# Kernel tuning notes

Measured on AMD Instinct MI355X. Metric: run time of the kernel, lower is better.

## Reference

```python
import jax, jax.numpy as jnp
import numpy as np

BN_EPS = 1e-5
NORM_EPS = 1e-12


def setup_inputs() -> dict:
    key = jax.random.key(0)
    ks = jax.random.split(key, 7)
    B, N, D, K, G = 64, 2048, 512, 64, 16
    init_sc = 1.0 / np.sqrt(D)
    return {
        "x": jax.random.normal(ks[0], (B, N, D), dtype=jnp.float32),
        "clusters": init_sc * jax.random.normal(ks[1], (D, K + G), dtype=jnp.float32),
        "clusters2": init_sc * jax.random.normal(ks[2], (1, D, K), dtype=jnp.float32),
        "bn_weight": jax.random.uniform(ks[3], (K + G,), dtype=jnp.float32, minval=0.5, maxval=1.5),
        "bn_bias": 0.1 * jax.random.normal(ks[4], (K + G,), dtype=jnp.float32),
        "running_mean": 0.1 * jax.random.normal(ks[5], (K + G,), dtype=jnp.float32),
        "running_var": jax.random.uniform(ks[6], (K + G,), dtype=jnp.float32, minval=0.5, maxval=1.5),
    }


def reference(x, clusters, clusters2, bn_weight, bn_bias, running_mean, running_var):
    # x: [B, N, D]; clusters: [D, K+G]; clusters2: [1, D, K]
    K = clusters2.shape[-1]
    # fused projection + BN (inference/affine form) + softmax over all K+G clusters
    scale = bn_weight * jax.lax.rsqrt(running_var + BN_EPS)          # [K+G]
    logits = jnp.einsum("bnd,dk->bnk", x, clusters)                  # [B, N, K+G]
    logits = (logits - running_mean) * scale + bn_bias
    assignment = jax.nn.softmax(logits, axis=-1)[..., :K]            # [B, N, K]
    # VLAD aggregation
    a_sum = jnp.sum(assignment, axis=1, keepdims=True)               # [B, 1, K]
    a = a_sum.transpose(0, 2, 1)[:, None, :, 0] * 0                  # placeholder avoided; compute directly below
    a = a_sum * clusters2.transpose(0, 2, 1)[..., None][..., 0].transpose(0, 2, 1) if False else a_sum.swapaxes(1, 2)[..., None][..., 0]  # not used
    a = jnp.einsum("bok,odk->bdk", a_sum, clusters2)                 # [B, D, K]
    vlad = jnp.einsum("bnd,bnk->bdk", x, assignment) - a             # [B, D, K]
    # intra-normalize over D
    vlad = vlad / jnp.maximum(jnp.linalg.norm(vlad, axis=1, keepdims=True), NORM_EPS)
    vlad = vlad.reshape(vlad.shape[0], -1)                           # [B, D*K]
    vlad = vlad / jnp.maximum(jnp.linalg.norm(vlad, axis=-1, keepdims=True), NORM_EPS)
    return vlad
```

## Files before the change

kernel.cpp:

```cpp
#include <hip/hip_runtime.h>
#include <hip/hip_bf16.h>
#include <math.h>
#include <string.h>

#define BN 131072

typedef __attribute__((ext_vector_type(8))) short bf16x8;
typedef __attribute__((ext_vector_type(4))) float f32x4;

__device__ __forceinline__ unsigned short f2bf(float f) {
    unsigned int u = __float_as_uint(f);
    u += 0x7fffu + ((u >> 16) & 1u);
    return (unsigned short)(u >> 16);
}

__device__ __forceinline__ unsigned int pk_bf16(float a, float b) {
    __hip_bfloat162 h = __float22bfloat162_rn(float2{a, b});
    unsigned int u;
    memcpy(&u, &h, 4);
    return u;
}

__global__ __launch_bounds__(256) void prep(
    const float* __restrict__ clusters, const float* __restrict__ bnw,
    const float* __restrict__ bnb, const float* __restrict__ rm,
    const float* __restrict__ rv,
    unsigned short* __restrict__ cT, float* __restrict__ bnadd)
{
    int i = blockIdx.x * 256 + threadIdx.x;
    int d = i / 80;
    int kg = i - d * 80;
    float mul = bnw[kg] * rsqrtf(rv[kg] + 1e-5f);
    cT[kg * 512 + d] = f2bf(clusters[i] * mul);
    if (i < 80) bnadd[i] = bnb[i] - rm[i] * mul;
}

__global__ __launch_bounds__(256) void pass_a(
    const float* __restrict__ x, const unsigned short* __restrict__ cT,
    const float* __restrict__ bnadd,
    unsigned short* __restrict__ assignT, float* __restrict__ a_sum)
{
    __shared__ unsigned short xs[64 * 136];
    __shared__ unsigned short cs[80 * 136];

    const int tid = threadIdx.x;
    const int w = tid >> 6, lane = tid & 63;
    const int q = lane >> 4, m = lane & 15;
    const int rowbase = blockIdx.x * 64;
    const int b = rowbase >> 11;

    f32x4 acc[5];
#pragma unroll
    for (int t = 0; t < 5; ++t) acc[t] = (f32x4){0.f, 0.f, 0.f, 0.f};

    for (int c = 0; c < 4; ++c) {
#pragma unroll
        for (int r = 0; r < 8; ++r) {
            int i = tid + 256 * r;
            int row = i >> 5, dd = (i & 31) * 4;
            float4 v = *(const float4*)(x + (size_t)(rowbase + row) * 512 + c * 128 + dd);
            uint2 p = { pk_bf16(v.x, v.y), pk_bf16(v.z, v.w) };
            *(uint2*)&xs[row * 136 + dd] = p;
        }
#pragma unroll
        for (int r = 0; r < 10; ++r) {
            int i = tid + 256 * r;
            int kg = i >> 5, dd = (i & 31) * 4;
            *(ushort4*)&cs[kg * 136 + dd] = *(const ushort4*)(cT + kg * 512 + c * 128 + dd);
        }
        __syncthreads();
#pragma unroll
        for (int ks = 0; ks < 4; ++ks) {
            bf16x8 a = *(const bf16x8*)&xs[(w * 16 + m) * 136 + ks * 32 + q * 8];
#pragma unroll
            for (int t = 0; t < 5; ++t) {
                bf16x8 bb = *(const bf16x8*)&cs[(m + 16 * t) * 136 + ks * 32 + q * 8];
                acc[t] = __builtin_amdgcn_mfma_f32_16x16x32_bf16(a, bb, acc[t], 0, 0, 0);
            }
        }
        __syncthreads();
    }

    float addv[5];
#pragma unroll
    for (int t = 0; t < 5; ++t) addv[t] = bnadd[m + 16 * t];

    float e[5][4], rs4[4];
#pragma unroll
    for (int i = 0; i < 4; ++i) {
        float v[5];
#pragma unroll
        for (int t = 0; t < 5; ++t) v[t] = acc[t][i] + addv[t];
        float mx = v[0];
#pragma unroll
        for (int t = 1; t < 5; ++t) mx = fmaxf(mx, v[t]);
        mx = fmaxf(mx, __shfl_xor(mx, 1, 64));
        mx = fmaxf(mx, __shfl_xor(mx, 2, 64));
        mx = fmaxf(mx, __shfl_xor(mx, 4, 64));
        mx = fmaxf(mx, __shfl_xor(mx, 8, 64));
        float sum = 0.f;
#pragma unroll
        for (int t = 0; t < 5; ++t) { e[t][i] = __expf(v[t] - mx); sum += e[t][i]; }
        sum += __shfl_xor(sum, 1, 64);
        sum += __shfl_xor(sum, 2, 64);
        sum += __shfl_xor(sum, 4, 64);
        sum += __shfl_xor(sum, 8, 64);
        rs4[i] = 1.0f / sum;
    }

    const int n0 = rowbase + w * 16 + q * 4;
#pragma unroll
    for (int t = 0; t < 4; ++t) {
        float a0 = e[t][0] * rs4[0], a1 = e[t][1] * rs4[1];
        float a2 = e[t][2] * rs4[2], a3 = e[t][3] * rs4[3];
        uint2 h = { pk_bf16(a0, a1), pk_bf16(a2, a3) };
        *(uint2*)(assignT + (size_t)(m + 16 * t) * BN + n0) = h;
        float as = a0 + a1 + a2 + a3;
        as += __shfl_xor(as, 16, 64);
        as += __shfl_xor(as, 32, 64);
        if (lane < 16) atomicAdd(&a_sum[b * 64 + m + 16 * t], as);
    }
}

__global__ __launch_bounds__(256) void pass_b(
    const float* __restrict__ x, const unsigned short* __restrict__ assignT,
    const float* __restrict__ a_sum, const float* __restrict__ clusters2,
    float* __restrict__ vlad, float* __restrict__ colssq)
{
    __shared__ unsigned short xs2[64 * 130];
    __shared__ unsigned short as2[64 * 72];

    const int tid = threadIdx.x;
    const int w = tid >> 6, lane = tid & 63;
    const int q = lane >> 4, m = lane & 15;
    const int dt = blockIdx.x;
    const int b = blockIdx.y;

    f32x4 acc[4];
#pragma unroll
    for (int t = 0; t < 4; ++t) acc[t] = (f32x4){0.f, 0.f, 0.f, 0.f};

    for (int nc = 0; nc < 2048; nc += 64) {
#pragma unroll
        for (int r = 0; r < 4; ++r) {
            int i = tid + 256 * r;
            int nl = i >> 4, dd = (i & 15) * 4;
            float4 v = *(const float4*)(x + (size_t)(b * 2048 + nc + nl) * 512 + dt * 64 + dd);
            *(unsigned int*)&xs2[nl * 130 + dd]     = pk_bf16(v.x, v.y);
            *(unsigned int*)&xs2[nl * 130 + dd + 2] = pk_bf16(v.z, v.w);
        }
#pragma unroll
        for (int r = 0; r < 4; ++r) {
            int i = tid + 256 * r;
            int kc = i >> 4, nl4 = (i & 15) * 4;
            *(ushort4*)&as2[kc * 72 + nl4] =
                *(const ushort4*)(assignT + (size_t)kc * BN + b * 2048 + nc + nl4);
        }
        __syncthreads();
#pragma unroll
        for (int ks = 0; ks < 2; ++ks) {
            union { unsigned short u[8]; bf16x8 v; } af;
            const int dcol = w * 16 + m;
#pragma unroll
            for (int j = 0; j < 8; ++j)
                af.u[j] = xs2[(ks * 32 + q * 8 + j) * 130 + dcol];
#pragma unroll
            for (int nt = 0; nt < 4; ++nt) {
                bf16x8 bb = *(const bf16x8*)&as2[(nt * 16 + m) * 72 + ks * 32 + q * 8];
                acc[nt] = __builtin_amdgcn_mfma_f32_16x16x32_bf16(af.v, bb, acc[nt], 0, 0, 0);
            }
        }
        __syncthreads();
    }

    const int d0 = dt * 64 + w * 16 + q * 4;
#pragma unroll
    for (int nt = 0; nt < 4; ++nt) {
        int kc = nt * 16 + m;
        float asv = a_sum[b * 64 + kc];
        float ss = 0.f;
#pragma unroll
        for (int i = 0; i < 4; ++i) {
            int d = d0 + i;
            float v = acc[nt][i] - asv * clusters2[d * 64 + kc];
            vlad[((size_t)b * 512 + d) * 64 + kc] = v;
            ss += v * v;
        }
        ss += __shfl_xor(ss, 16, 64);
        ss += __shfl_xor(ss, 32, 64);
        if (lane < 16) atomicAdd(&colssq[b * 64 + kc], ss);
    }
}

__global__ __launch_bounds__(256) void pass_c(
    const float* __restrict__ vlad, const float* __restrict__ colssq,
    float* __restrict__ out)
{
    __shared__ float sc[65];
    const int b = blockIdx.y, seg = blockIdx.x, tid = threadIdx.x;

    if (tid < 64) {
        float css = colssq[b * 64 + tid];
        float invc = 1.0f / fmaxf(sqrtf(css), 1e-12f);
        sc[tid] = invc;
        float ns = css * invc * invc;
        ns += __shfl_xor(ns, 1, 64);
        ns += __shfl_xor(ns, 2, 64);
        ns += __shfl_xor(ns, 4, 64);
        ns += __shfl_xor(ns, 8, 64);
        ns += __shfl_xor(ns, 16, 64);
        ns += __shfl_xor(ns, 32, 64);
        if (tid == 0) sc[64] = 1.0f / fmaxf(sqrtf(ns), 1e-12f);
    }
    __syncthreads();
    const float invr = sc[64];

#pragma unroll
    for (int r = 0; r < 4; ++r) {
        int i4 = seg * 1024 + r * 256 + tid;
        float4 v = *(const float4*)(vlad + (size_t)b * 32768 + (size_t)i4 * 4);
        int c0 = (i4 & 15) * 4;
        float4 o;
        o.x = v.x * sc[c0 + 0] * invr;
        o.y = v.y * sc[c0 + 1] * invr;
        o.z = v.z * sc[c0 + 2] * invr;
        o.w = v.w * sc[c0 + 3] * invr;
        *(float4*)(out + (size_t)b * 32768 + (size_t)i4 * 4) = o;
    }
}

extern "C" void kernel_launch(void* const* d_in, const int* in_sizes, int n_in,
                              void* d_out, int out_size, void* d_ws, size_t ws_size,
                              hipStream_t stream)
{
    const float* x         = (const float*)d_in[0];
    const float* clusters  = (const float*)d_in[1];
    const float* clusters2 = (const float*)d_in[2];
    const float* bn_w      = (const float*)d_in[3];
    const float* bn_b      = (const float*)d_in[4];
    const float* rmean     = (const float*)d_in[5];
    const float* rvar      = (const float*)d_in[6];
    float* out = (float*)d_out;

    char* ws = (char*)d_ws;
    float* a_sum            = (float*)(ws + 0);
    float* colssq           = (float*)(ws + 16384);
    float* bnadd            = (float*)(ws + 32768);
    unsigned short* cT      = (unsigned short*)(ws + 65536);
    unsigned short* assignT = (unsigned short*)(ws + 262144);
    float* vlad             = (float*)(ws + 262144 + 16777216);

    hipMemsetAsync(ws, 0, 32768, stream);

    prep<<<160, 256, 0, stream>>>(clusters, bn_w, bn_b, rmean, rvar, cT, bnadd);
    pass_a<<<2048, 256, 0, stream>>>(x, cT, bnadd, assignT, a_sum);
    pass_b<<<dim3(8, 64), 256, 0, stream>>>(x, assignT, a_sum, clusters2, vlad, colssq);
    pass_c<<<dim3(8, 64), 256, 0, stream>>>(vlad, colssq, out);
}
```

Baseline: 527.8 us.

## Prefetch next tiles into registers and split pass_b over N with partial reduction

Both GEMM passes now load the next chunk of x and cluster/assignment data into registers while the current chunk is consumed from shared memory, so global load latency overlaps with MFMA work. pass_b is split into two N-halves via a z grid dimension, which doubles the block count from 512 to 1024 for better occupancy on the GPU. The halves write partial results to a new workspace buffer. A new pass_c1 kernel sums the two partials, writes vlad and accumulates column sums of squares. This adds one kernel launch, extra partial-buffer traffic, and higher register pressure from the prefetch arrays.

Result: faster. 449.8 us (-14.8%).

```diff
diff --git a/kernel.cpp b/kernel.cpp
--- a/kernel.cpp
+++ b/kernel.cpp
@@ -53,22 +53,53 @@
 #pragma unroll
     for (int t = 0; t < 5; ++t) acc[t] = (f32x4){0.f, 0.f, 0.f, 0.f};
 
+    float4  vx[8];
+    ushort4 vc[10];
+
+#pragma unroll
+    for (int r = 0; r < 8; ++r) {
+        int i = tid + 256 * r;
+        int row = i >> 5, dd = (i & 31) * 4;
+        vx[r] = *(const float4*)(x + (size_t)(rowbase + row) * 512 + dd);
+    }
+#pragma unroll
+    for (int r = 0; r < 10; ++r) {
+        int i = tid + 256 * r;
+        int kg = i >> 5, dd = (i & 31) * 4;
+        vc[r] = *(const ushort4*)(cT + kg * 512 + dd);
+    }
+
     for (int c = 0; c < 4; ++c) {
 #pragma unroll
         for (int r = 0; r < 8; ++r) {
             int i = tid + 256 * r;
             int row = i >> 5, dd = (i & 31) * 4;
-            float4 v = *(const float4*)(x + (size_t)(rowbase + row) * 512 + c * 128 + dd);
-            uint2 p = { pk_bf16(v.x, v.y), pk_bf16(v.z, v.w) };
+            uint2 p = { pk_bf16(vx[r].x, vx[r].y), pk_bf16(vx[r].z, vx[r].w) };
             *(uint2*)&xs[row * 136 + dd] = p;
         }
 #pragma unroll
         for (int r = 0; r < 10; ++r) {
             int i = tid + 256 * r;
             int kg = i >> 5, dd = (i & 31) * 4;
-            *(ushort4*)&cs[kg * 136 + dd] = *(const ushort4*)(cT + kg * 512 + c * 128 + dd);
+            *(ushort4*)&cs[kg * 136 + dd] = vc[r];
         }
         __syncthreads();
+
+        if (c < 3) {
+#pragma unroll
+            for (int r = 0; r < 8; ++r) {
+                int i = tid + 256 * r;
+                int row = i >> 5, dd = (i & 31) * 4;
+                vx[r] = *(const float4*)(x + (size_t)(rowbase + row) * 512 + (c + 1) * 128 + dd);
+            }
+#pragma unroll
+            for (int r = 0; r < 10; ++r) {
+                int i = tid + 256 * r;
+                int kg = i >> 5, dd = (i & 31) * 4;
+                vc[r] = *(const ushort4*)(cT + kg * 512 + (c + 1) * 128 + dd);
+            }
+        }
+
 #pragma unroll
         for (int ks = 0; ks < 4; ++ks) {
             bf16x8 a = *(const bf16x8*)&xs[(w * 16 + m) * 136 + ks * 32 + q * 8];
@@ -125,7 +156,7 @@
 __global__ __launch_bounds__(256) void pass_b(
     const float* __restrict__ x, const unsigned short* __restrict__ assignT,
     const float* __restrict__ a_sum, const float* __restrict__ clusters2,
-    float* __restrict__ vlad, float* __restrict__ colssq)
+    float* __restrict__ part)
 {
     __shared__ unsigned short xs2[64 * 130];
     __shared__ unsigned short as2[64 * 72];
@@ -135,28 +166,60 @@
     const int q = lane >> 4, m = lane & 15;
     const int dt = blockIdx.x;
     const int b = blockIdx.y;
+    const int ns = blockIdx.z;
+    const int nbase = ns * 1024;
 
     f32x4 acc[4];
 #pragma unroll
     for (int t = 0; t < 4; ++t) acc[t] = (f32x4){0.f, 0.f, 0.f, 0.f};
 
-    for (int nc = 0; nc < 2048; nc += 64) {
+    float4  vx[4];
+    ushort4 va[4];
+
+#pragma unroll
+    for (int r = 0; r < 4; ++r) {
+        int i = tid + 256 * r;
+        int nl = i >> 4, dd = (i & 15) * 4;
+        vx[r] = *(const float4*)(x + (size_t)(b * 2048 + nbase + nl) * 512 + dt * 64 + dd);
+    }
+#pragma unroll
+    for (int r = 0; r < 4; ++r) {
+        int i = tid + 256 * r;
+        int kc = i >> 4, nl4 = (i & 15) * 4;
+        va[r] = *(const ushort4*)(assignT + (size_t)kc * BN + b * 2048 + nbase + nl4);
+    }
+
+    for (int nc = nbase; nc < nbase + 1024; nc += 64) {
 #pragma unroll
         for (int r = 0; r < 4; ++r) {
             int i = tid + 256 * r;
             int nl = i >> 4, dd = (i & 15) * 4;
-            float4 v = *(const float4*)(x + (size_t)(b * 2048 + nc + nl) * 512 + dt * 64 + dd);
-            *(unsigned int*)&xs2[nl * 130 + dd]     = pk_bf16(v.x, v.y);
-            *(unsigned int*)&xs2[nl * 130 + dd + 2] = pk_bf16(v.z, v.w);
+            *(unsigned int*)&xs2[nl * 130 + dd]     = pk_bf16(vx[r].x, vx[r].y);
+            *(unsigned int*)&xs2[nl * 130 + dd + 2] = pk_bf16(vx[r].z, vx[r].w);
         }
 #pragma unroll
         for (int r = 0; r < 4; ++r) {
             int i = tid + 256 * r;
             int kc = i >> 4, nl4 = (i & 15) * 4;
-            *(ushort4*)&as2[kc * 72 + nl4] =
-                *(const ushort4*)(assignT + (size_t)kc * BN + b * 2048 + nc + nl4);
+            *(ushort4*)&as2[kc * 72 + nl4] = va[r];
         }
         __syncthreads();
+
+        if (nc + 64 < nbase + 1024) {
+#pragma unroll
+            for (int r = 0; r < 4; ++r) {
+                int i = tid + 256 * r;
+                int nl = i >> 4, dd = (i & 15) * 4;
+                vx[r] = *(const float4*)(x + (size_t)(b * 2048 + nc + 64 + nl) * 512 + dt * 64 + dd);
+            }
+#pragma unroll
+            for (int r = 0; r < 4; ++r) {
+                int i = tid + 256 * r;
+                int kc = i >> 4, nl4 = (i & 15) * 4;
+                va[r] = *(const ushort4*)(assignT + (size_t)kc * BN + b * 2048 + nc + 64 + nl4);
+            }
+        }
+
 #pragma unroll
         for (int ks = 0; ks < 2; ++ks) {
             union { unsigned short u[8]; bf16x8 v; } af;
@@ -173,26 +236,47 @@
         __syncthreads();
     }
 
+    float* dst = part + (size_t)ns * (64 * 512 * 64);
     const int d0 = dt * 64 + w * 16 + q * 4;
 #pragma unroll
     for (int nt = 0; nt < 4; ++nt) {
         int kc = nt * 16 + m;
-        float asv = a_sum[b * 64 + kc];
-        float ss = 0.f;
+        float asv = (ns == 0) ? a_sum[b * 64 + kc] : 0.f;
 #pragma unroll
         for (int i = 0; i < 4; ++i) {
             int d = d0 + i;
             float v = acc[nt][i] - asv * clusters2[d * 64 + kc];
-            vlad[((size_t)b * 512 + d) * 64 + kc] = v;
-            ss += v * v;
-        }
-        ss += __shfl_xor(ss, 16, 64);
-        ss += __shfl_xor(ss, 32, 64);
-        if (lane < 16) atomicAdd(&colssq[b * 64 + kc], ss);
-    }
-}
-
-__global__ __launch_bounds__(256) void pass_c(
+            dst[((size_t)b * 512 + d) * 64 + kc] = v;
+        }
+    }
+}
+
+__global__ __launch_bounds__(256) void pass_c1(
+    const float* __restrict__ part, float* __restrict__ vlad,
+    float* __restrict__ colssq)
+{
+    __shared__ float red[256];
+    const int b = blockIdx.y, seg = blockIdx.x, tid = threadIdx.x;
+    const int k = tid & 63, dg = tid >> 6;
+    const float* p0 = part;
+    const float* p1 = part + (size_t)(64 * 512 * 64);
+
+    float ssq = 0.f;
+#pragma unroll
+    for (int j = 0; j < 16; ++j) {
+        int d = seg * 64 + dg + j * 4;
+        size_t idx = ((size_t)b * 512 + d) * 64 + k;
+        float v = p0[idx] + p1[idx];
+        vlad[idx] = v;
+        ssq += v * v;
+    }
+    red[tid] = ssq;
+    __syncthreads();
+    if (tid < 64)
+        atomicAdd(&colssq[b * 64 + k], red[k] + red[64 + k] + red[128 + k] + red[192 + k]);
+}
+
+__global__ __launch_bounds__(256) void pass_c2(
     const float* __restrict__ vlad, const float* __restrict__ colssq,
     float* __restrict__ out)
 {
@@ -249,11 +333,13 @@
     unsigned short* cT      = (unsigned short*)(ws + 65536);
     unsigned short* assignT = (unsigned short*)(ws + 262144);
     float* vlad             = (float*)(ws + 262144 + 16777216);
+    float* part             = (float*)(ws + 262144 + 16777216 + 8388608);
 
     hipMemsetAsync(ws, 0, 32768, stream);
 
     prep<<<160, 256, 0, stream>>>(clusters, bn_w, bn_b, rmean, rvar, cT, bnadd);
     pass_a<<<2048, 256, 0, stream>>>(x, cT, bnadd, assignT, a_sum);
-    pass_b<<<dim3(8, 64), 256, 0, stream>>>(x, assignT, a_sum, clusters2, vlad, colssq);
-    pass_c<<<dim3(8, 64), 256, 0, stream>>>(vlad, colssq, out);
-}
+    pass_b<<<dim3(8, 64, 2), 256, 0, stream>>>(x, assignT, a_sum, clusters2, part);
+    pass_c1<<<dim3(8, 64), 256, 0, stream>>>(part, vlad, colssq);
+    pass_c2<<<dim3(8, 64), 256, 0, stream>>>(vlad, colssq, out);
+}
```
